# Optimization experiments

Measured on AMD Instinct MI355X. Metric: run time of the kernel, lower is better.

The kernel has to match this reference:

```python
import jax, jax.numpy as jnp
from jax import lax
import numpy as np

VOCAB = 32000
EMB = 256
UNITS = 1024
STEPS = 128
START_TOKEN = 1


def setup_inputs() -> dict:
    key = jax.random.key(0)
    ks = jax.random.split(key, 7)
    B, Hf, Wf, C = 32, 8, 25, 512
    s = 0.02
    return {
        "image_encoding": jax.random.normal(ks[0], (B, Hf, Wf, C), jnp.float32),
        "embedding": jax.random.normal(ks[1], (VOCAB, EMB), jnp.float32) * s,
        "lstm_kernel": jax.random.normal(ks[2], (EMB + C, 4 * UNITS), jnp.float32) * s,
        "lstm_rec_kernel": jax.random.normal(ks[3], (UNITS, 4 * UNITS), jnp.float32) * s,
        "lstm_bias": jnp.zeros((4 * UNITS,), jnp.float32),
        "proj_w": jax.random.normal(ks[4], (UNITS, VOCAB), jnp.float32) * s,
        "proj_b": jnp.zeros((VOCAB,), jnp.float32),
    }


def _lstm_cell(x, h, c, K, R, b):
    # Keras LSTMCell: gate order i, f, c, o; sigmoid gates, tanh cell.
    z = x @ K + h @ R + b  # [B, 4*UNITS]
    zi, zf, zc, zo = jnp.split(z, 4, axis=-1)
    i = jax.nn.sigmoid(zi)
    f = jax.nn.sigmoid(zf)
    o = jax.nn.sigmoid(zo)
    c_new = f * c + i * jnp.tanh(zc)
    h_new = o * jnp.tanh(c_new)
    return h_new, c_new


def reference(image_encoding, embedding, lstm_kernel, lstm_rec_kernel, lstm_bias, proj_w, proj_b):
    B = image_encoding.shape[0]
    C = image_encoding.shape[-1]
    # flatten_image_features=False -> mean over spatial positions
    features = image_encoding.reshape(B, -1, C).mean(axis=1)  # [B, C]

    start_emb = jnp.tile(embedding[START_TOKEN][None, :], (B, 1))  # [B, EMB]
    h0 = jnp.zeros((B, UNITS), features.dtype)
    c0 = jnp.zeros((B, UNITS), features.dtype)
    key0 = jax.random.key(42)

    def step(carry, _):
        h, c, inp, key = carry
        key, sub = jax.random.split(key)
        x = jnp.concatenate([inp, features], axis=-1)  # augment(inp)
        h, c = _lstm_cell(x, h, c, lstm_kernel, lstm_rec_kernel, lstm_bias)
        logits = h @ proj_w + proj_b  # [B, VOCAB]
        samples = jax.random.categorical(sub, logits)  # [B] int
        inp = embedding[samples]  # [B, EMB]
        return (h, c, inp, key), samples

    _, samples = lax.scan(step, (h0, c0, start_emb, key0), None, length=STEPS)
    # samples: [STEPS, B] -> [B, STEPS] as in tf.transpose(convert_to_tensor(output))
    return samples.T
```

## Files before the change

kernel.cpp:

```cpp
#include <hip/hip_runtime.h>
#include <cstdint>
#include <cstddef>


#define VOCAB 32000
#define EMB 256
#define UNITS 1024
#define STEPS 128
#define BATCH 32
#define XROWS 768
#define TINYF 1.17549435e-38f

typedef uint32_t u32x16 __attribute__((ext_vector_type(16)));

__host__ __device__ __forceinline__ void tf2x32(uint32_t k0, uint32_t k1,
                                                uint32_t x0, uint32_t x1,
                                                uint32_t& o0, uint32_t& o1) {
  uint32_t ks2 = k0 ^ k1 ^ 0x1BD11BDAu;
#define TFR(r) { x0 += x1; x1 = (x1 << (r)) | (x1 >> (32 - (r))); x1 ^= x0; }
  x0 += k0; x1 += k1;
  TFR(13) TFR(15) TFR(26) TFR(6)  x0 += k1;  x1 += ks2 + 1u;
  TFR(17) TFR(29) TFR(16) TFR(24) x0 += ks2; x1 += k0 + 2u;
  TFR(13) TFR(15) TFR(26) TFR(6)  x0 += k0;  x1 += k1 + 3u;
  TFR(17) TFR(29) TFR(16) TFR(24) x0 += k1;  x1 += ks2 + 4u;
  TFR(13) TFR(15) TFR(26) TFR(6)  x0 += ks2; x1 += k0 + 5u;
#undef TFR
  o0 = x0; o1 = x1;
}

__device__ __forceinline__ void sload_b(const float* p, u32x16& a, u32x16& b) {
  asm volatile("s_load_dwordx16 %0, %2, 0x0\n\t"
               "s_load_dwordx16 %1, %2, 0x40\n\t"
               "s_waitcnt lgkmcnt(0)"
               : "=&s"(a), "=&s"(b)
               : "s"(p));
}

__device__ __forceinline__ void fma32(float* acc, float w,
                                      const u32x16& xa, const u32x16& xb) {
#pragma unroll
  for (int b = 0; b < 16; ++b)
    acc[b] = fmaf(w, __uint_as_float(xa[b]), acc[b]);
#pragma unroll
  for (int b = 0; b < 16; ++b)
    acc[b + 16] = fmaf(w, __uint_as_float(xb[b]), acc[b + 16]);
}

__global__ __launch_bounds__(256) void k_init(
    const float* __restrict__ img, const float* __restrict__ emb,
    float* __restrict__ xT, float* __restrict__ h0, float* __restrict__ cT,
    unsigned long long* __restrict__ winners, unsigned int* __restrict__ cntA,
    unsigned int* __restrict__ cntB) {
  int idx = blockIdx.x * 256 + threadIdx.x;
  if (idx < 16384) {
    int b = idx >> 9, ch = idx & 511;
    const float* p = img + (size_t)b * 102400 + ch;
    float s = 0.f;
    for (int t = 0; t < 200; ++t) s += p[(size_t)t * 512];
    xT[(size_t)(256 + ch) * 32 + b] = s / 200.0f;
  } else if (idx < 24576) {
    int i2 = idx - 16384;
    int e = i2 >> 5, b = i2 & 31;
    xT[(size_t)e * 32 + b] = emb[256 + e];
  } else if (idx < 57344) {
    h0[idx - 24576] = 0.f;
  } else if (idx < 90112) {
    cT[idx - 57344] = 0.f;
  } else if (idx < 94208) {
    winners[idx - 90112] = 0ull;
  } else if (idx < 96256) {
    cntA[idx - 94208] = 0u;
  } else if (idx < 96384) {
    cntB[idx - 96256] = 0u;
  }
}

__global__ __launch_bounds__(512) void k_lstm(
    const float* __restrict__ Km, const float* __restrict__ Rm,
    const float* __restrict__ bias, const float* __restrict__ xT,
    const float* __restrict__ hr, float* __restrict__ hw,
    float* __restrict__ cT, float* __restrict__ zpart,
    unsigned int* cntA, int t) {
  const int tid = threadIdx.x;
  const int lane = tid & 63;
  const int strip = __builtin_amdgcn_readfirstlane(tid >> 6);
  const int jt = blockIdx.x >> 3;
  const int e = blockIdx.x & 7;
  const int j = jt * 64 + lane;
  const int m = jt & 15;

  __shared__ float red[4][64][33];
  __shared__ int lastf;

  float acc[32];
#pragma unroll
  for (int b = 0; b < 32; ++b) acc[b] = 0.f;

  const int klo = e * 224 + strip * 28;
  const int khi = klo + 28;

  float wc = (klo < XROWS) ? Km[(size_t)klo * 4096 + j]
                           : Rm[(size_t)(klo - XROWS) * 4096 + j];
  for (int k = klo; k < khi; ++k) {
    float wn = 0.f;
    int kn = k + 1;
    if (kn < khi)
      wn = (kn < XROWS) ? Km[(size_t)kn * 4096 + j]
                        : Rm[(size_t)(kn - XROWS) * 4096 + j];
    const float* xrow = (k < XROWS) ? (xT + (size_t)k * 32)
                                    : (hr + (size_t)(k - XROWS) * 32);
    u32x16 xa, xb;
    sload_b(xrow, xa, xb);
    fma32(acc, wc, xa, xb);
    wc = wn;
  }

  if (strip < 4) {
#pragma unroll
    for (int b = 0; b < 32; ++b) red[strip][lane][b] = acc[b];
  }
  __syncthreads();
  if (strip >= 4) {
#pragma unroll
    for (int b = 0; b < 32; ++b) red[strip - 4][lane][b] += acc[b];
  }
  __syncthreads();

#pragma unroll
  for (int it = 0; it < 4; ++it) {
    int idx = it * 512 + tid;
    int col = idx >> 5, b = idx & 31;
    float s = ((red[0][col][b] + red[1][col][b]) + red[2][col][b]) +
              red[3][col][b];
    zpart[((size_t)e * 4096 + jt * 64 + col) * 32 + b] = s;
  }
  __syncthreads();
  if (tid == 0) {
    __threadfence();
    unsigned int old = atomicAdd(&cntA[t * 16 + m], 1u);
    lastf = (old == 31u);
  }
  __syncthreads();

  if (lastf) {
    __threadfence();
#pragma unroll
    for (int it = 0; it < 4; ++it) {
      int idx = it * 512 + tid;
      int ul = idx >> 5, b = idx & 31;
      int u = m * 64 + ul;
      float zs[4];
#pragma unroll
      for (int g = 0; g < 4; ++g) {
        int jj = g * 1024 + u;
        const float* zp = zpart + (size_t)jj * 32 + b;
        float s = zp[0];
#pragma unroll
        for (int ee = 1; ee < 8; ++ee) s += zp[(size_t)ee * 4096 * 32];
        zs[g] = s + bias[jj];
      }
      float ig = 1.0f / (1.0f + expf(-zs[0]));
      float fg = 1.0f / (1.0f + expf(-zs[1]));
      float og = 1.0f / (1.0f + expf(-zs[3]));
      float cold = cT[(size_t)u * 32 + b];
      float cn = fg * cold + ig * tanhf(zs[2]);
      cT[(size_t)u * 32 + b] = cn;
      hw[(size_t)u * 32 + b] = og * tanhf(cn);
    }
  }
}

__global__ __launch_bounds__(512) void k_logits(
    const float* __restrict__ Pw, const float* __restrict__ pb,
    const float* __restrict__ emb, const float* __restrict__ hr,
    float* __restrict__ xT, unsigned long long* winners,
    unsigned int* cntB, int* __restrict__ out, int t, uint32_t s0,
    uint32_t s1) {
  const int tid = threadIdx.x;
  const int lane = tid & 63;
  const int strip = __builtin_amdgcn_readfirstlane(tid >> 6);
  const int v0 = blockIdx.x * 64;

  __shared__ float red[4][64][33];
  __shared__ unsigned long long wbs[32][17];
  __shared__ int samp[BATCH];
  __shared__ int lastf;

  float acc[32];
#pragma unroll
  for (int b = 0; b < 32; ++b) acc[b] = 0.f;

  {
    const float* xp = hr + (size_t)(strip * 128) * 32;
    const float* wp = Pw + (size_t)(strip * 128) * VOCAB + v0 + lane;
    float wc0 = wp[0], wc1 = wp[VOCAB], wc2 = wp[2 * VOCAB],
          wc3 = wp[3 * VOCAB];
    const float* wpp = wp + (size_t)4 * VOCAB;
    u32x16 xa, xb;
    for (int k = 0; k < 124; k += 4) {
      float wn0 = wpp[0], wn1 = wpp[VOCAB], wn2 = wpp[2 * VOCAB],
            wn3 = wpp[3 * VOCAB];
      wpp += (size_t)4 * VOCAB;
      sload_b(xp, xa, xb); xp += 32; fma32(acc, wc0, xa, xb);
      sload_b(xp, xa, xb); xp += 32; fma32(acc, wc1, xa, xb);
      sload_b(xp, xa, xb); xp += 32; fma32(acc, wc2, xa, xb);
      sload_b(xp, xa, xb); xp += 32; fma32(acc, wc3, xa, xb);
      wc0 = wn0; wc1 = wn1; wc2 = wn2; wc3 = wn3;
    }
    sload_b(xp, xa, xb); xp += 32; fma32(acc, wc0, xa, xb);
    sload_b(xp, xa, xb); xp += 32; fma32(acc, wc1, xa, xb);
    sload_b(xp, xa, xb); xp += 32; fma32(acc, wc2, xa, xb);
    sload_b(xp, xa, xb);           fma32(acc, wc3, xa, xb);
  }

  if (strip < 4) {
#pragma unroll
    for (int b = 0; b < 32; ++b) red[strip][lane][b] = acc[b];
  }
  __syncthreads();
  if (strip >= 4) {
#pragma unroll
    for (int b = 0; b < 32; ++b) red[strip - 4][lane][b] += acc[b];
  }
  __syncthreads();

#pragma unroll
  for (int it = 0; it < 4; ++it) {
    int idx = it * 512 + tid;
    int col = idx >> 5, b = idx & 31;
    float s = ((red[0][col][b] + red[1][col][b]) + red[2][col][b]) +
              red[3][col][b] + pb[v0 + col];
    red[0][col][b] = s;
  }
  __syncthreads();

  {
    const int b = tid & 31;
    const int sub = tid >> 5;
    unsigned long long best = 0ull;
#pragma unroll
    for (int c = 0; c < 4; ++c) {
      int col = sub * 4 + c;
      int vv = v0 + col;
      float logit = red[0][col][b];
      uint32_t y0, y1;
      tf2x32(s0, s1, 0u, (uint32_t)(b * VOCAB + vv), y0, y1);
      uint32_t bits = y0 ^ y1;
      uint32_t fb = (bits >> 9) | 0x3F800000u;
      float f = __uint_as_float(fb) - 1.0f;
      float u = f + TINYF;
      u = fmaxf(TINYF, u);
      float g = -logf(-logf(u));
      float val = g + logit;
      uint32_t ub = __float_as_uint(val);
      ub = ((int)ub < 0) ? ~ub : (ub | 0x80000000u);
      unsigned long long pk =
          ((unsigned long long)ub << 32) | (uint32_t)(~(uint32_t)vv);
      if (pk > best) best = pk;
    }
    wbs[b][sub] = best;
  }
  __syncthreads();

  if (tid < 32) {
    unsigned long long best = wbs[tid][0];
#pragma unroll
    for (int s = 1; s < 16; ++s)
      best = (wbs[tid][s] > best) ? wbs[tid][s] : best;
    unsigned long long cur = winners[t * 32 + tid];
    if (best > cur) atomicMax(&winners[t * 32 + tid], best);
  }
  __syncthreads();
  if (tid == 0) {
    __threadfence();
    unsigned int old = atomicAdd(&cntB[t], 1u);
    lastf = (old == 499u);
  }
  __syncthreads();

  if (lastf) {
    __threadfence();
    if (tid < 32) {
      unsigned long long w = atomicMax(&winners[t * 32 + tid], 0ull);
      int vv = (int)(~(uint32_t)(w & 0xFFFFFFFFull));
      samp[tid] = vv;
      out[tid * STEPS + t] = vv;
    }
    __syncthreads();
#pragma unroll
    for (int it = 0; it < 16; ++it) {
      int idx = it * 512 + tid;
      int b = idx >> 8, e2 = idx & 255;
      xT[(size_t)e2 * 32 + b] = emb[(size_t)samp[b] * EMB + e2];
    }
  }
}

extern "C" void kernel_launch(void* const* d_in, const int* in_sizes, int n_in,
                              void* d_out, int out_size, void* d_ws,
                              size_t ws_size, hipStream_t stream) {
  (void)in_sizes; (void)n_in; (void)out_size; (void)ws_size;
  const float* img  = (const float*)d_in[0];
  const float* emb  = (const float*)d_in[1];
  const float* Km   = (const float*)d_in[2];
  const float* Rm   = (const float*)d_in[3];
  const float* bias = (const float*)d_in[4];
  const float* Pw   = (const float*)d_in[5];
  const float* pb   = (const float*)d_in[6];
  int* out = (int*)d_out;

  char* ws = (char*)d_ws;
  unsigned long long* winners = (unsigned long long*)(ws + 0);
  unsigned int* cntA = (unsigned int*)(ws + 32768);
  unsigned int* cntB = (unsigned int*)(ws + 40960);
  float* xT   = (float*)(ws + 49152);
  float* hb0  = (float*)(ws + 147456);
  float* hb1  = (float*)(ws + 278528);
  float* cT   = (float*)(ws + 409600);
  float* zpart = (float*)(ws + 540672);

  k_init<<<377, 256, 0, stream>>>(img, emb, xT, hb0, cT, winners, cntA, cntB);

  uint32_t k0 = 0u, k1 = 42u;
  for (int t = 0; t < STEPS; ++t) {
    uint32_t n0, n1, su0, su1;
    tf2x32(k0, k1, 0u, 0u, n0, n1);
    tf2x32(k0, k1, 0u, 1u, su0, su1);
    k0 = n0; k1 = n1;

    const float* hrd = (t & 1) ? hb1 : hb0;
    float* hwr = (t & 1) ? hb0 : hb1;
    k_lstm<<<512, 512, 0, stream>>>(Km, Rm, bias, xT, hrd, hwr, cT, zpart,
                                    cntA, t);
    k_logits<<<500, 512, 0, stream>>>(Pw, pb, emb, hwr, xT, winners, cntB,
                                      out, t, su0, su1);
  }
}
```

Baseline: 12.83 ms.

## Stage activation rows in LDS via async global-to-LDS loads instead of scalar loads

Both GEMV kernels stop loading the 32-wide activation rows with inline s_load_dwordx16 plus a full lgkmcnt wait per row. They now copy tiles of activations into double-buffered shared memory with global_load_lds and read them back as float4, and batch the weight loads per tile (7 or 16 rows per strip). The logits kernel places this buffer in a union with its reduction scratch, and both kernels get a min-blocks-per-CU launch bound. The aim is to remove the serialising scalar-load waits and expose more memory-level parallelism, at the cost of extra barriers per tile and possible register-pressure or spill effects from the occupancy hint.

```diff
diff --git a/kernel.cpp b/kernel.cpp
--- a/kernel.cpp
+++ b/kernel.cpp
@@ -10,8 +10,6 @@
 #define BATCH 32
 #define XROWS 768
 #define TINYF 1.17549435e-38f
-
-typedef uint32_t u32x16 __attribute__((ext_vector_type(16)));
 
 __host__ __device__ __forceinline__ void tf2x32(uint32_t k0, uint32_t k1,
                                                 uint32_t x0, uint32_t x1,
@@ -28,22 +26,10 @@
   o0 = x0; o1 = x1;
 }
 
-__device__ __forceinline__ void sload_b(const float* p, u32x16& a, u32x16& b) {
-  asm volatile("s_load_dwordx16 %0, %2, 0x0\n\t"
-               "s_load_dwordx16 %1, %2, 0x40\n\t"
-               "s_waitcnt lgkmcnt(0)"
-               : "=&s"(a), "=&s"(b)
-               : "s"(p));
-}
-
-__device__ __forceinline__ void fma32(float* acc, float w,
-                                      const u32x16& xa, const u32x16& xb) {
-#pragma unroll
-  for (int b = 0; b < 16; ++b)
-    acc[b] = fmaf(w, __uint_as_float(xa[b]), acc[b]);
-#pragma unroll
-  for (int b = 0; b < 16; ++b)
-    acc[b + 16] = fmaf(w, __uint_as_float(xb[b]), acc[b + 16]);
+__device__ __forceinline__ void gld_lds16(const float* g, float* l) {
+  __builtin_amdgcn_global_load_lds(
+      (const __attribute__((address_space(1))) void*)(g),
+      (__attribute__((address_space(3))) void*)(l), 16, 0, 0);
 }
 
 __global__ __launch_bounds__(256) void k_init(
@@ -75,7 +61,7 @@
   }
 }
 
-__global__ __launch_bounds__(512) void k_lstm(
+__global__ __launch_bounds__(512, 4) void k_lstm(
     const float* __restrict__ Km, const float* __restrict__ Rm,
     const float* __restrict__ bias, const float* __restrict__ xT,
     const float* __restrict__ hr, float* __restrict__ hw,
@@ -88,7 +74,9 @@
   const int e = blockIdx.x & 7;
   const int j = jt * 64 + lane;
   const int m = jt & 15;
-
+  const int R0 = e * 224;
+
+  __shared__ float xs[2][56][32];
   __shared__ float red[4][64][33];
   __shared__ int lastf;
 
@@ -96,23 +84,48 @@
 #pragma unroll
   for (int b = 0; b < 32; ++b) acc[b] = 0.f;
 
-  const int klo = e * 224 + strip * 28;
-  const int khi = klo + 28;
-
-  float wc = (klo < XROWS) ? Km[(size_t)klo * 4096 + j]
-                           : Rm[(size_t)(klo - XROWS) * 4096 + j];
-  for (int k = klo; k < khi; ++k) {
-    float wn = 0.f;
-    int kn = k + 1;
-    if (kn < khi)
-      wn = (kn < XROWS) ? Km[(size_t)kn * 4096 + j]
-                        : Rm[(size_t)(kn - XROWS) * 4096 + j];
-    const float* xrow = (k < XROWS) ? (xT + (size_t)k * 32)
-                                    : (hr + (size_t)(k - XROWS) * 32);
-    u32x16 xa, xb;
-    sload_b(xrow, xa, xb);
-    fma32(acc, wc, xa, xb);
-    wc = wn;
+  if (strip < 7) {
+    const int slot = strip * 64 + lane;
+    const int row = slot >> 3, c4 = (slot & 7) * 4;
+    const int g = R0 + row;
+    const float* src = (g < XROWS) ? (xT + (size_t)g * 32 + c4)
+                                   : (hr + (size_t)(g - XROWS) * 32 + c4);
+    gld_lds16(src, &xs[0][0][0] + strip * 256);
+  }
+
+  for (int p = 0; p < 4; ++p) {
+    __syncthreads();
+    if (p < 3 && strip < 7) {
+      const int slot = strip * 64 + lane;
+      const int row = slot >> 3, c4 = (slot & 7) * 4;
+      const int g = R0 + (p + 1) * 56 + row;
+      const float* src = (g < XROWS) ? (xT + (size_t)g * 32 + c4)
+                                     : (hr + (size_t)(g - XROWS) * 32 + c4);
+      gld_lds16(src, &xs[(p + 1) & 1][0][0] + strip * 256);
+    }
+    float w[7];
+#pragma unroll
+    for (int i = 0; i < 7; ++i) {
+      const int g = R0 + p * 56 + strip * 7 + i;
+      w[i] = (g < XROWS) ? Km[(size_t)g * 4096 + j]
+                         : Rm[(size_t)(g - XROWS) * 4096 + j];
+    }
+    const int buf = p & 1;
+#pragma unroll
+    for (int i = 0; i < 7; ++i) {
+      const float4* xr =
+          reinterpret_cast<const float4*>(&xs[buf][strip * 7 + i][0]);
+      float4 xv[8];
+#pragma unroll
+      for (int c = 0; c < 8; ++c) xv[c] = xr[c];
+#pragma unroll
+      for (int c = 0; c < 8; ++c) {
+        acc[4 * c + 0] = fmaf(w[i], xv[c].x, acc[4 * c + 0]);
+        acc[4 * c + 1] = fmaf(w[i], xv[c].y, acc[4 * c + 1]);
+        acc[4 * c + 2] = fmaf(w[i], xv[c].z, acc[4 * c + 2]);
+        acc[4 * c + 3] = fmaf(w[i], xv[c].w, acc[4 * c + 3]);
+      }
+    }
   }
 
   if (strip < 4) {
@@ -170,7 +183,7 @@
   }
 }
 
-__global__ __launch_bounds__(512) void k_logits(
+__global__ __launch_bounds__(512, 4) void k_logits(
     const float* __restrict__ Pw, const float* __restrict__ pb,
     const float* __restrict__ emb, const float* __restrict__ hr,
     float* __restrict__ xT, unsigned long long* winners,
@@ -181,9 +194,14 @@
   const int strip = __builtin_amdgcn_readfirstlane(tid >> 6);
   const int v0 = blockIdx.x * 64;
 
-  __shared__ float red[4][64][33];
-  __shared__ unsigned long long wbs[32][17];
-  __shared__ int samp[BATCH];
+  __shared__ union {
+    float xs[2][128][32];
+    struct {
+      float red[4][64][33];
+      unsigned long long wbs[32][17];
+      int samp[BATCH];
+    } r;
+  } sh;
   __shared__ int lastf;
 
   float acc[32];
@@ -191,36 +209,53 @@
   for (int b = 0; b < 32; ++b) acc[b] = 0.f;
 
   {
-    const float* xp = hr + (size_t)(strip * 128) * 32;
-    const float* wp = Pw + (size_t)(strip * 128) * VOCAB + v0 + lane;
-    float wc0 = wp[0], wc1 = wp[VOCAB], wc2 = wp[2 * VOCAB],
-          wc3 = wp[3 * VOCAB];
-    const float* wpp = wp + (size_t)4 * VOCAB;
-    u32x16 xa, xb;
-    for (int k = 0; k < 124; k += 4) {
-      float wn0 = wpp[0], wn1 = wpp[VOCAB], wn2 = wpp[2 * VOCAB],
-            wn3 = wpp[3 * VOCAB];
-      wpp += (size_t)4 * VOCAB;
-      sload_b(xp, xa, xb); xp += 32; fma32(acc, wc0, xa, xb);
-      sload_b(xp, xa, xb); xp += 32; fma32(acc, wc1, xa, xb);
-      sload_b(xp, xa, xb); xp += 32; fma32(acc, wc2, xa, xb);
-      sload_b(xp, xa, xb); xp += 32; fma32(acc, wc3, xa, xb);
-      wc0 = wn0; wc1 = wn1; wc2 = wn2; wc3 = wn3;
-    }
-    sload_b(xp, xa, xb); xp += 32; fma32(acc, wc0, xa, xb);
-    sload_b(xp, xa, xb); xp += 32; fma32(acc, wc1, xa, xb);
-    sload_b(xp, xa, xb); xp += 32; fma32(acc, wc2, xa, xb);
-    sload_b(xp, xa, xb);           fma32(acc, wc3, xa, xb);
-  }
+    const int c0 = strip * 2;
+    gld_lds16(hr + (size_t)c0 * 256 + lane * 4, &sh.xs[0][0][0] + c0 * 256);
+    gld_lds16(hr + (size_t)(c0 + 1) * 256 + lane * 4,
+              &sh.xs[0][0][0] + (c0 + 1) * 256);
+  }
+
+  for (int p = 0; p < 8; ++p) {
+    __syncthreads();
+    if (p < 7) {
+      const int c0 = strip * 2;
+      const float* src = hr + (size_t)(p + 1) * 4096;
+      float* dst = &sh.xs[(p + 1) & 1][0][0];
+      gld_lds16(src + (size_t)c0 * 256 + lane * 4, dst + c0 * 256);
+      gld_lds16(src + (size_t)(c0 + 1) * 256 + lane * 4, dst + (c0 + 1) * 256);
+    }
+    const float* wp = Pw + (size_t)(p * 128 + strip * 16) * VOCAB + v0 + lane;
+    float w[16];
+#pragma unroll
+    for (int i = 0; i < 16; ++i) w[i] = wp[(size_t)i * VOCAB];
+    const int buf = p & 1;
+#pragma unroll
+    for (int i = 0; i < 16; ++i) {
+      const float4* xr =
+          reinterpret_cast<const float4*>(&sh.xs[buf][strip * 16 + i][0]);
+      float4 xv[8];
+#pragma unroll
+      for (int c = 0; c < 8; ++c) xv[c] = xr[c];
+#pragma unroll
+      for (int c = 0; c < 8; ++c) {
+        acc[4 * c + 0] = fmaf(w[i], xv[c].x, acc[4 * c + 0]);
+        acc[4 * c + 1] = fmaf(w[i], xv[c].y, acc[4 * c + 1]);
+        acc[4 * c + 2] = fmaf(w[i], xv[c].z, acc[4 * c + 2]);
+        acc[4 * c + 3] = fmaf(w[i], xv[c].w, acc[4 * c + 3]);
+      }
+    }
+  }
+
+  __syncthreads();
 
   if (strip < 4) {
 #pragma unroll
-    for (int b = 0; b < 32; ++b) red[strip][lane][b] = acc[b];
+    for (int b = 0; b < 32; ++b) sh.r.red[strip][lane][b] = acc[b];
   }
   __syncthreads();
   if (strip >= 4) {
 #pragma unroll
-    for (int b = 0; b < 32; ++b) red[strip - 4][lane][b] += acc[b];
+    for (int b = 0; b < 32; ++b) sh.r.red[strip - 4][lane][b] += acc[b];
   }
   __syncthreads();
 
@@ -228,9 +263,10 @@
   for (int it = 0; it < 4; ++it) {
     int idx = it * 512 + tid;
     int col = idx >> 5, b = idx & 31;
-    float s = ((red[0][col][b] + red[1][col][b]) + red[2][col][b]) +
-              red[3][col][b] + pb[v0 + col];
-    red[0][col][b] = s;
+    float s = ((sh.r.red[0][col][b] + sh.r.red[1][col][b]) +
+               sh.r.red[2][col][b]) +
+              sh.r.red[3][col][b] + pb[v0 + col];
+    sh.r.red[0][col][b] = s;
   }
   __syncthreads();
 
@@ -242,7 +278,7 @@
     for (int c = 0; c < 4; ++c) {
       int col = sub * 4 + c;
       int vv = v0 + col;
-      float logit = red[0][col][b];
+      float logit = sh.r.red[0][col][b];
       uint32_t y0, y1;
       tf2x32(s0, s1, 0u, (uint32_t)(b * VOCAB + vv), y0, y1);
       uint32_t bits = y0 ^ y1;
@@ -258,15 +294,15 @@
           ((unsigned long long)ub << 32) | (uint32_t)(~(uint32_t)vv);
       if (pk > best) best = pk;
     }
-    wbs[b][sub] = best;
+    sh.r.wbs[b][sub] = best;
   }
   __syncthreads();
 
   if (tid < 32) {
-    unsigned long long best = wbs[tid][0];
+    unsigned long long best = sh.r.wbs[tid][0];
 #pragma unroll
     for (int s = 1; s < 16; ++s)
-      best = (wbs[tid][s] > best) ? wbs[tid][s] : best;
+      best = (sh.r.wbs[tid][s] > best) ? sh.r.wbs[tid][s] : best;
     unsigned long long cur = winners[t * 32 + tid];
     if (best > cur) atomicMax(&winners[t * 32 + tid], best);
   }
@@ -283,7 +319,7 @@
     if (tid < 32) {
       unsigned long long w = atomicMax(&winners[t * 32 + tid], 0ull);
       int vv = (int)(~(uint32_t)(w & 0xFFFFFFFFull));
-      samp[tid] = vv;
+      sh.r.samp[tid] = vv;
       out[tid * STEPS + t] = vv;
     }
     __syncthreads();
@@ -291,7 +327,7 @@
     for (int it = 0; it < 16; ++it) {
       int idx = it * 512 + tid;
       int b = idx >> 8, e2 = idx & 255;
-      xT[(size_t)e2 * 32 + b] = emb[(size_t)samp[b] * EMB + e2];
+      xT[(size_t)e2 * 32 + b] = emb[(size_t)sh.r.samp[b] * EMB + e2];
     }
   }
 }
```

Result: slower. 43.59 ms (+239.7%).

## Replace scalar-load broadcast GEMV with 8x4 register tiles and vector loads

Applied to the files above, without the earlier changes.

In both the LSTM and logits kernels, the per-lane mapping changes. Before, each lane owned one output column and read all 32 batch values through scalar s_load_dwordx16 broadcasts, waiting on each load. Now each lane owns an 8-column by 4-batch register tile and fetches weights and activations with float4 vector loads, software-pipelined one row ahead. This removes the serialized scalar-load waits and spreads activation loads across vector memory. The cost is more vector load traffic for activations and LDS stores with a strided pattern that may cause bank conflicts.

```diff
diff --git a/kernel.cpp b/kernel.cpp
--- a/kernel.cpp
+++ b/kernel.cpp
@@ -10,8 +10,6 @@
 #define BATCH 32
 #define XROWS 768
 #define TINYF 1.17549435e-38f
-
-typedef uint32_t u32x16 __attribute__((ext_vector_type(16)));
 
 __host__ __device__ __forceinline__ void tf2x32(uint32_t k0, uint32_t k1,
                                                 uint32_t x0, uint32_t x1,
@@ -28,22 +26,17 @@
   o0 = x0; o1 = x1;
 }
 
-__device__ __forceinline__ void sload_b(const float* p, u32x16& a, u32x16& b) {
-  asm volatile("s_load_dwordx16 %0, %2, 0x0\n\t"
-               "s_load_dwordx16 %1, %2, 0x40\n\t"
-               "s_waitcnt lgkmcnt(0)"
-               : "=&s"(a), "=&s"(b)
-               : "s"(p));
-}
-
-__device__ __forceinline__ void fma32(float* acc, float w,
-                                      const u32x16& xa, const u32x16& xb) {
-#pragma unroll
-  for (int b = 0; b < 16; ++b)
-    acc[b] = fmaf(w, __uint_as_float(xa[b]), acc[b]);
-#pragma unroll
-  for (int b = 0; b < 16; ++b)
-    acc[b + 16] = fmaf(w, __uint_as_float(xb[b]), acc[b + 16]);
+__device__ __forceinline__ void fma_8x4(float* acc, const float4& wa,
+                                        const float4& wb, const float4& x) {
+  const float w8[8] = {wa.x, wa.y, wa.z, wa.w, wb.x, wb.y, wb.z, wb.w};
+#pragma unroll
+  for (int c = 0; c < 8; ++c) {
+    float wv = w8[c];
+    acc[c * 4 + 0] = fmaf(wv, x.x, acc[c * 4 + 0]);
+    acc[c * 4 + 1] = fmaf(wv, x.y, acc[c * 4 + 1]);
+    acc[c * 4 + 2] = fmaf(wv, x.z, acc[c * 4 + 2]);
+    acc[c * 4 + 3] = fmaf(wv, x.w, acc[c * 4 + 3]);
+  }
 }
 
 __global__ __launch_bounds__(256) void k_init(
@@ -86,7 +79,8 @@
   const int strip = __builtin_amdgcn_readfirstlane(tid >> 6);
   const int jt = blockIdx.x >> 3;
   const int e = blockIdx.x & 7;
-  const int j = jt * 64 + lane;
+  const int cs = lane >> 3;
+  const int bg = lane & 7;
   const int m = jt & 15;
 
   __shared__ float red[4][64][33];
@@ -97,32 +91,41 @@
   for (int b = 0; b < 32; ++b) acc[b] = 0.f;
 
   const int klo = e * 224 + strip * 28;
-  const int khi = klo + 28;
-
-  float wc = (klo < XROWS) ? Km[(size_t)klo * 4096 + j]
-                           : Rm[(size_t)(klo - XROWS) * 4096 + j];
-  for (int k = klo; k < khi; ++k) {
-    float wn = 0.f;
-    int kn = k + 1;
-    if (kn < khi)
-      wn = (kn < XROWS) ? Km[(size_t)kn * 4096 + j]
-                        : Rm[(size_t)(kn - XROWS) * 4096 + j];
-    const float* xrow = (k < XROWS) ? (xT + (size_t)k * 32)
-                                    : (hr + (size_t)(k - XROWS) * 32);
-    u32x16 xa, xb;
-    sload_b(xrow, xa, xb);
-    fma32(acc, wc, xa, xb);
-    wc = wn;
-  }
+  const int wcol = jt * 64 + cs * 8;
+
+#define XROW(k) ((k) < XROWS ? (xT + (size_t)(k) * 32) \
+                             : (hr + (size_t)((k) - XROWS) * 32))
+#define WROW(k) ((k) < XROWS ? (Km + (size_t)(k) * 4096) \
+                             : (Rm + (size_t)((k) - XROWS) * 4096))
+  float4 xc = *reinterpret_cast<const float4*>(XROW(klo) + bg * 4);
+  float4 wa = *reinterpret_cast<const float4*>(WROW(klo) + wcol);
+  float4 wb = *reinterpret_cast<const float4*>(WROW(klo) + wcol + 4);
+  for (int i = 0; i < 27; ++i) {
+    const int kn = klo + i + 1;
+    float4 xn = *reinterpret_cast<const float4*>(XROW(kn) + bg * 4);
+    float4 wan = *reinterpret_cast<const float4*>(WROW(kn) + wcol);
+    float4 wbn = *reinterpret_cast<const float4*>(WROW(kn) + wcol + 4);
+    fma_8x4(acc, wa, wb, xc);
+    xc = xn; wa = wan; wb = wbn;
+  }
+  fma_8x4(acc, wa, wb, xc);
+#undef XROW
+#undef WROW
 
   if (strip < 4) {
 #pragma unroll
-    for (int b = 0; b < 32; ++b) red[strip][lane][b] = acc[b];
+    for (int c = 0; c < 8; ++c)
+#pragma unroll
+      for (int bb = 0; bb < 4; ++bb)
+        red[strip][cs * 8 + c][bg * 4 + bb] = acc[c * 4 + bb];
   }
   __syncthreads();
   if (strip >= 4) {
 #pragma unroll
-    for (int b = 0; b < 32; ++b) red[strip - 4][lane][b] += acc[b];
+    for (int c = 0; c < 8; ++c)
+#pragma unroll
+      for (int bb = 0; bb < 4; ++bb)
+        red[strip - 4][cs * 8 + c][bg * 4 + bb] += acc[c * 4 + bb];
   }
   __syncthreads();
 
@@ -180,6 +183,8 @@
   const int lane = tid & 63;
   const int strip = __builtin_amdgcn_readfirstlane(tid >> 6);
   const int v0 = blockIdx.x * 64;
+  const int cs = lane >> 3;
+  const int bg = lane & 7;
 
   __shared__ float red[4][64][33];
   __shared__ unsigned long long wbs[32][17];
@@ -191,36 +196,36 @@
   for (int b = 0; b < 32; ++b) acc[b] = 0.f;
 
   {
-    const float* xp = hr + (size_t)(strip * 128) * 32;
-    const float* wp = Pw + (size_t)(strip * 128) * VOCAB + v0 + lane;
-    float wc0 = wp[0], wc1 = wp[VOCAB], wc2 = wp[2 * VOCAB],
-          wc3 = wp[3 * VOCAB];
-    const float* wpp = wp + (size_t)4 * VOCAB;
-    u32x16 xa, xb;
-    for (int k = 0; k < 124; k += 4) {
-      float wn0 = wpp[0], wn1 = wpp[VOCAB], wn2 = wpp[2 * VOCAB],
-            wn3 = wpp[3 * VOCAB];
-      wpp += (size_t)4 * VOCAB;
-      sload_b(xp, xa, xb); xp += 32; fma32(acc, wc0, xa, xb);
-      sload_b(xp, xa, xb); xp += 32; fma32(acc, wc1, xa, xb);
-      sload_b(xp, xa, xb); xp += 32; fma32(acc, wc2, xa, xb);
-      sload_b(xp, xa, xb); xp += 32; fma32(acc, wc3, xa, xb);
-      wc0 = wn0; wc1 = wn1; wc2 = wn2; wc3 = wn3;
-    }
-    sload_b(xp, xa, xb); xp += 32; fma32(acc, wc0, xa, xb);
-    sload_b(xp, xa, xb); xp += 32; fma32(acc, wc1, xa, xb);
-    sload_b(xp, xa, xb); xp += 32; fma32(acc, wc2, xa, xb);
-    sload_b(xp, xa, xb);           fma32(acc, wc3, xa, xb);
+    const float* xp = hr + (size_t)(strip * 128) * 32 + bg * 4;
+    const float* wp = Pw + (size_t)(strip * 128) * VOCAB + v0 + cs * 8;
+    float4 xc = *reinterpret_cast<const float4*>(xp);
+    float4 wa = *reinterpret_cast<const float4*>(wp);
+    float4 wb = *reinterpret_cast<const float4*>(wp + 4);
+    for (int k = 0; k < 127; ++k) {
+      float4 xn = *reinterpret_cast<const float4*>(xp + 32);
+      float4 wan = *reinterpret_cast<const float4*>(wp + VOCAB);
+      float4 wbn = *reinterpret_cast<const float4*>(wp + VOCAB + 4);
+      xp += 32; wp += VOCAB;
+      fma_8x4(acc, wa, wb, xc);
+      xc = xn; wa = wan; wb = wbn;
+    }
+    fma_8x4(acc, wa, wb, xc);
   }
 
   if (strip < 4) {
 #pragma unroll
-    for (int b = 0; b < 32; ++b) red[strip][lane][b] = acc[b];
+    for (int c = 0; c < 8; ++c)
+#pragma unroll
+      for (int bb = 0; bb < 4; ++bb)
+        red[strip][cs * 8 + c][bg * 4 + bb] = acc[c * 4 + bb];
   }
   __syncthreads();
   if (strip >= 4) {
 #pragma unroll
-    for (int b = 0; b < 32; ++b) red[strip - 4][lane][b] += acc[b];
+    for (int c = 0; c < 8; ++c)
+#pragma unroll
+      for (int bb = 0; bb < 4; ++bb)
+        red[strip - 4][cs * 8 + c][bg * 4 + bb] += acc[c * 4 + bb];
   }
   __syncthreads();
 
```

Result: slower. 14.05 ms (+9.5%).
